# Kernel tuning notes

Measured on AMD Instinct MI355X. Metric: run time of the kernel, lower is better.

The kernel has to match this reference:

```python
import jax, jax.numpy as jnp
import numpy as np

HIDDEN = 2048
HEAD_DIM = 128
GROUPS = 8
HEADS = HIDDEN // HEAD_DIM          # 16
HPG = HEADS // GROUPS               # heads per group = 2


def setup_inputs() -> dict:
    key = jax.random.key(0)
    ks = jax.random.split(key, 9)
    b, sl, sk = 2, 2048, 2048
    s = 0.02
    return {
        "q": jax.random.normal(ks[0], (b, sl, HIDDEN), jnp.float32),
        "k": jax.random.normal(ks[1], (b, sk, HIDDEN), jnp.float32),
        "v": jax.random.normal(ks[2], (b, sk, HIDDEN), jnp.float32),
        "Wq": jax.random.normal(ks[3], (HIDDEN, HIDDEN), jnp.float32) * s,
        "bq": jax.random.normal(ks[4], (HIDDEN,), jnp.float32) * s,
        "Wk": jax.random.normal(ks[5], (HIDDEN, HEAD_DIM * GROUPS), jnp.float32) * s,
        "bk": jax.random.normal(ks[6], (HEAD_DIM * GROUPS,), jnp.float32) * s,
        "Wv": jax.random.normal(ks[7], (HIDDEN, HEAD_DIM * GROUPS), jnp.float32) * s,
        "bv": jax.random.normal(ks[8], (HEAD_DIM * GROUPS,), jnp.float32) * s,
    }


def reference(q, k, v, Wq, bq, Wk, bk, Wv, bv):
    b, sl, _ = q.shape
    sk = k.shape[1]
    qp = q @ Wq + bq                                   # [b, sl, hidden]
    kp = k @ Wk + bk                                   # [b, sk, G*d]
    vp = v @ Wv + bv                                   # [b, sk, G*d]
    # head h = g*HPG + j uses group g, matching torch repeat_interleave on dim=1
    qh = qp.reshape(b, sl, GROUPS, HPG, HEAD_DIM).transpose(0, 2, 3, 1, 4)  # [b,G,hpg,sl,d]
    kh = kp.reshape(b, sk, GROUPS, HEAD_DIM).transpose(0, 2, 1, 3)          # [b,G,sk,d]
    vh = vp.reshape(b, sk, GROUPS, HEAD_DIM).transpose(0, 2, 1, 3)          # [b,G,sk,d]
    scale = 1.0 / jnp.sqrt(jnp.asarray(HEAD_DIM, qh.dtype))
    score = jnp.einsum("bghld,bgsd->bghls", qh, kh) * scale                 # [b,G,hpg,sl,sk]
    attn = jax.nn.softmax(score, axis=-1)
    out = jnp.einsum("bghls,bgsd->bghld", attn, vh)                         # [b,G,hpg,sl,d]
    out = out.transpose(0, 3, 1, 2, 4).reshape(b, sl, HIDDEN)
    return out
```

## Files before the change

### kernel.cpp

```cpp
#include <hip/hip_runtime.h>

typedef unsigned short u16;
typedef short v8s __attribute__((ext_vector_type(8)));
typedef float v4f __attribute__((ext_vector_type(4)));
typedef float v16f __attribute__((ext_vector_type(16)));

typedef __attribute__((address_space(3))) u16* lptr_t;
typedef const __attribute__((address_space(1))) void* gptr_t;

__device__ __forceinline__ u16 f2b(float f) {
  unsigned int u = __float_as_uint(f);
  u += 0x7fff + ((u >> 16) & 1);
  return (u16)(u >> 16);
}

__global__ __launch_bounds__(256) void conv3_bf16(const float* __restrict__ q,
                                                  const float* __restrict__ k,
                                                  const float* __restrict__ v,
                                                  u16* __restrict__ qd,
                                                  u16* __restrict__ kd,
                                                  u16* __restrict__ vd) {
  int blk = blockIdx.x;
  const float* s; u16* d;
  if (blk < 4096)      { s = q; d = qd; }
  else if (blk < 8192) { s = k; d = kd; blk -= 4096; }
  else                 { s = v; d = vd; blk -= 8192; }
  int i = (blk * 256 + threadIdx.x) * 8;
  float4 a = *(const float4*)&s[i];
  float4 b = *(const float4*)&s[i + 4];
  union { uint4 v4; u16 u[8]; } p;
  p.u[0] = f2b(a.x); p.u[1] = f2b(a.y); p.u[2] = f2b(a.z); p.u[3] = f2b(a.w);
  p.u[4] = f2b(b.x); p.u[5] = f2b(b.y); p.u[6] = f2b(b.z); p.u[7] = f2b(b.w);
  *(uint4*)&d[i] = p.v4;
}

__global__ __launch_bounds__(256) void transp3_w(const float* __restrict__ Wq,
                                                 const float* __restrict__ Wk,
                                                 const float* __restrict__ Wv,
                                                 u16* __restrict__ wt) {
  __shared__ u16 tile[64][65];
  int blk = blockIdx.x;
  const float* W; int N; u16* dst;
  if (blk < 1024)      { W = Wq; N = 2048; dst = wt; }
  else if (blk < 1536) { W = Wk; N = 1024; dst = wt + (size_t)2048 * 2048; blk -= 1024; }
  else                 { W = Wv; N = 1024; dst = wt + (size_t)3072 * 2048; blk -= 1536; }
  const int k0 = (blk & 31) * 64;
  const int n0 = (blk >> 5) * 64;
  const int t = threadIdx.x;
#pragma unroll
  for (int i = 0; i < 2; ++i) {
    int chunk = i * 256 + t;
    int kr = chunk >> 3;
    int nc = (chunk & 7) * 8;
    float4 a = *(const float4*)&W[(size_t)(k0 + kr) * N + n0 + nc];
    float4 b = *(const float4*)&W[(size_t)(k0 + kr) * N + n0 + nc + 4];
    tile[kr][nc + 0] = f2b(a.x); tile[kr][nc + 1] = f2b(a.y);
    tile[kr][nc + 2] = f2b(a.z); tile[kr][nc + 3] = f2b(a.w);
    tile[kr][nc + 4] = f2b(b.x); tile[kr][nc + 5] = f2b(b.y);
    tile[kr][nc + 6] = f2b(b.z); tile[kr][nc + 7] = f2b(b.w);
  }
  __syncthreads();
#pragma unroll
  for (int i = 0; i < 2; ++i) {
    int chunk = i * 256 + t;
    int nr = chunk >> 3;
    int kc = (chunk & 7) * 8;
    union { uint4 v; u16 u[8]; } cv;
#pragma unroll
    for (int j = 0; j < 8; ++j) cv.u[j] = tile[kc + j][nr];
    *(uint4*)&dst[(size_t)(n0 + nr) * 2048 + k0 + kc] = cv.v;
  }
}

__global__ __launch_bounds__(256) void qkv_gemm(const u16* __restrict__ qbf,
                                                const u16* __restrict__ kbf,
                                                const u16* __restrict__ vbf,
                                                const u16* __restrict__ wt_all,
                                                const float* __restrict__ bq,
                                                const float* __restrict__ bk,
                                                const float* __restrict__ bv,
                                                u16* __restrict__ qp,
                                                u16* __restrict__ kp,
                                                u16* __restrict__ vpt) {
  __shared__ __align__(16) u16 A_sh[128 * 32];
  __shared__ __align__(16) u16 B_sh[128 * 32];
  const int m0 = blockIdx.x * 128;
  const int n0 = blockIdx.y * 128;
  const int t = threadIdx.x;
  const int wave = t >> 6, lane = t & 63;
  const int quad = lane >> 4, l16 = lane & 15;
  const int wm = (wave & 1) * 64, wn = (wave >> 1) * 64;

  const u16* Abase; const float* bias; int region, nloc0;
  if (n0 < 2048)      { Abase = qbf; bias = bq; region = 0; nloc0 = n0; }
  else if (n0 < 3072) { Abase = kbf; bias = bk; region = 1; nloc0 = n0 - 2048; }
  else                { Abase = vbf; bias = bv; region = 2; nloc0 = n0 - 3072; }

  const int st_r = lane >> 2;
  const int st_c = (lane & 3) * 8;
  const int seg = wave * 2;

  v4f acc[4][4] = {};

  for (int k0 = 0; k0 < 2048; k0 += 32) {
#pragma unroll
    for (int i = 0; i < 2; ++i) {
      int rows = (seg + i) * 16;
      const u16* ga = &Abase[(size_t)(m0 + rows + st_r) * 2048 + k0 + st_c];
      lptr_t la = (lptr_t)&A_sh[rows * 32] + lane * 8;
      __builtin_amdgcn_global_load_lds((gptr_t)ga,
                                       (__attribute__((address_space(3))) void*)la, 16, 0, 0);
      const u16* gb = &wt_all[(size_t)(n0 + rows + st_r) * 2048 + k0 + st_c];
      lptr_t lb = (lptr_t)&B_sh[rows * 32] + lane * 8;
      __builtin_amdgcn_global_load_lds((gptr_t)gb,
                                       (__attribute__((address_space(3))) void*)lb, 16, 0, 0);
    }
    __syncthreads();

    v8s af[4], bf[4];
#pragma unroll
    for (int i = 0; i < 4; ++i)
      af[i] = *(const v8s*)&A_sh[(wm + i * 16 + l16) * 32 + quad * 8];
#pragma unroll
    for (int j = 0; j < 4; ++j)
      bf[j] = *(const v8s*)&B_sh[(wn + j * 16 + l16) * 32 + quad * 8];
#pragma unroll
    for (int i = 0; i < 4; ++i)
#pragma unroll
      for (int j = 0; j < 4; ++j)
        acc[i][j] = __builtin_amdgcn_mfma_f32_16x16x32_bf16(af[i], bf[j], acc[i][j], 0, 0, 0);
    __syncthreads();
  }

#pragma unroll
  for (int j = 0; j < 4; ++j) {
    int nl = nloc0 + wn + j * 16 + l16;
    float bvl = bias[nl];
    if (region == 0) {
#pragma unroll
      for (int i = 0; i < 4; ++i)
#pragma unroll
        for (int r = 0; r < 4; ++r) {
          int m = m0 + wm + i * 16 + quad * 4 + r;
          qp[(size_t)m * 2048 + nl] = f2b((acc[i][j][r] + bvl) * 0.08838834764831845f);
        }
    } else if (region == 1) {
#pragma unroll
      for (int i = 0; i < 4; ++i)
#pragma unroll
        for (int r = 0; r < 4; ++r) {
          int m = m0 + wm + i * 16 + quad * 4 + r;
          kp[(size_t)m * 1024 + nl] = f2b(acc[i][j][r] + bvl);
        }
    } else {
      int g = nl >> 7, d = nl & 127;
#pragma unroll
      for (int i = 0; i < 4; ++i) {
        int mb = m0 + wm + i * 16 + quad * 4;
        int b = mb >> 11, s = mb & 2047;
        ushort4 pk;
        pk.x = f2b(acc[i][j][0] + bvl);
        pk.y = f2b(acc[i][j][1] + bvl);
        pk.z = f2b(acc[i][j][2] + bvl);
        pk.w = f2b(acc[i][j][3] + bvl);
        *(ushort4*)&vpt[(((size_t)b * 8 + g) * 128 + d) * 2048 + s] = pk;
      }
    }
  }
}

__global__ __launch_bounds__(256, 2) void gqa_attn2(const u16* __restrict__ qp,
                                                    const u16* __restrict__ kp,
                                                    const u16* __restrict__ vpt,
                                                    float* __restrict__ out) {
  __shared__ __align__(16) u16 K_sh[2][64 * 128];
  __shared__ __align__(16) u16 V_sh[2][128 * 64];

  const int qtile = blockIdx.x;
  const int head = blockIdx.y;
  const int batch = blockIdx.z;
  const int g = head >> 1;
  const int q0 = qtile * 128;

  const u16* qpb = qp + (size_t)batch * 2048 * 2048;
  const u16* kpb = kp + (size_t)batch * 2048 * 1024;
  const u16* vptb = vpt + (size_t)batch * 8 * 128 * 2048;
  float* outb = out + (size_t)batch * 2048 * 2048;

  const int t = threadIdx.x;
  const int wave = t >> 6, lane = t & 63;
  const int l = lane & 31, h = lane >> 5;

  v8s qf[8];
  {
    const u16* qrow = &qpb[(size_t)(q0 + wave * 32 + l) * 2048 + head * 128];
#pragma unroll
    for (int ks = 0; ks < 8; ++ks)
      qf[ks] = *(const v8s*)&qrow[ks * 16 + h * 8];
  }

  int colK[8];
#pragma unroll
  for (int ks = 0; ks < 8; ++ks) colK[ks] = ((2 * ks + h) ^ (l & 7)) * 8;

  int koff[4], voff[4];
#pragma unroll
  for (int i = 0; i < 4; ++i) {
    int krow = wave * 16 + i * 4 + (lane >> 4);
    int kg = (lane & 15) ^ (krow & 7);
    koff[i] = krow * 1024 + g * 128 + kg * 8;
    int vrow = wave * 32 + i * 8 + (lane >> 3);
    int vg = (lane & 7) ^ (vrow & 7);
    voff[i] = (g * 128 + vrow) * 2048 + vg * 8;
  }

#define STAGE_KV(BUF, S0)                                                               \
  do {                                                                                  \
    _Pragma("unroll") for (int i_ = 0; i_ < 4; ++i_) {                                  \
      const u16* gk_ = kpb + (size_t)(S0) * 1024 + koff[i_];                            \
      lptr_t lk_ = (lptr_t)&K_sh[BUF][(wave * 16 + i_ * 4) * 128] + lane * 8;           \
      __builtin_amdgcn_global_load_lds((gptr_t)gk_,                                     \
                                       (__attribute__((address_space(3))) void*)lk_,    \
                                       16, 0, 0);                                       \
      const u16* gv_ = vptb + voff[i_] + (S0);                                          \
      lptr_t lv_ = (lptr_t)&V_sh[BUF][(wave * 32 + i_ * 8) * 64] + lane * 8;            \
      __builtin_amdgcn_global_load_lds((gptr_t)gv_,                                     \
                                       (__attribute__((address_space(3))) void*)lv_,    \
                                       16, 0, 0);                                       \
    }                                                                                   \
  } while (0)

  v16f o_acc[4] = {};
  float rs = 0.0f;

  STAGE_KV(0, 0);
  __syncthreads();

  int cur = 0;
  for (int sc = 0; sc < 32; ++sc) {
    if (sc < 31) STAGE_KV(cur ^ 1, (sc + 1) * 64);

    v16f sacc[2] = {};
    __builtin_amdgcn_s_setprio(1);
#pragma unroll
    for (int kb = 0; kb < 2; ++kb)
#pragma unroll
      for (int ks = 0; ks < 8; ++ks) {
        v8s kf = *(const v8s*)&K_sh[cur][(kb * 32 + l) * 128 + colK[ks]];
        sacc[kb] = __builtin_amdgcn_mfma_f32_32x32x16_bf16(kf, qf[ks], sacc[kb], 0, 0, 0);
      }
    __builtin_amdgcn_s_setprio(0);

    unsigned int w[16];
#pragma unroll
    for (int kb = 0; kb < 2; ++kb)
#pragma unroll
      for (int p = 0; p < 8; ++p) {
        float e0 = __expf(sacc[kb][2 * p]);
        float e1 = __expf(sacc[kb][2 * p + 1]);
        rs += e0 + e1;
        asm("v_cvt_pk_bf16_f32 %0, %1, %2" : "=v"(w[kb * 8 + p]) : "v"(e0), "v"(e1));
      }

    v8s pa[4];
#pragma unroll
    for (int j = 0; j < 4; ++j) {
      unsigned int a = w[j * 4 + 0], c = w[j * 4 + 1];
      unsigned int b = w[j * 4 + 2], d = w[j * 4 + 3];
      asm("v_permlane32_swap_b32 %0, %1" : "+v"(a), "+v"(b));
      asm("v_permlane32_swap_b32 %0, %1" : "+v"(c), "+v"(d));
      union { unsigned int u[4]; v8s s; } pk;
      pk.u[0] = a; pk.u[1] = c; pk.u[2] = b; pk.u[3] = d;
      pa[j] = pk.s;
    }

    __builtin_amdgcn_s_setprio(1);
#pragma unroll
    for (int j = 0; j < 4; ++j)
#pragma unroll
      for (int db = 0; db < 4; ++db) {
        v8s vf = *(const v8s*)&V_sh[cur][(db * 32 + l) * 64 + colK[j]];
        o_acc[db] = __builtin_amdgcn_mfma_f32_32x32x16_bf16(pa[j], vf, o_acc[db], 0, 0, 0);
      }
    __builtin_amdgcn_s_setprio(0);

    __syncthreads();
    cur ^= 1;
  }

  float rst = rs + __shfl_xor(rs, 32, 64);
  float inv = 1.0f / rst;
#pragma unroll
  for (int r = 0; r < 16; ++r) {
    int qpat = (r & 3) + 8 * (r >> 2) + 4 * h;
    float invq = __shfl(inv, qpat, 64);
    int qrow = q0 + wave * 32 + qpat;
    float* orow = &outb[(size_t)qrow * 2048 + head * 128 + l];
#pragma unroll
    for (int db = 0; db < 4; ++db)
      orow[db * 32] = o_acc[db][r] * invq;
  }
#undef STAGE_KV
}

extern "C" void kernel_launch(void* const* d_in, const int* in_sizes, int n_in,
                              void* d_out, int out_size, void* d_ws, size_t ws_size,
                              hipStream_t stream) {
  const float* q  = (const float*)d_in[0];
  const float* k  = (const float*)d_in[1];
  const float* v  = (const float*)d_in[2];
  const float* Wq = (const float*)d_in[3];
  const float* bq = (const float*)d_in[4];
  const float* Wk = (const float*)d_in[5];
  const float* bk = (const float*)d_in[6];
  const float* Wv = (const float*)d_in[7];
  const float* bv = (const float*)d_in[8];
  float* out = (float*)d_out;
  char* ws = (char*)d_ws;

  u16* qbf    = (u16*)(ws + 0);
  u16* kbf    = (u16*)(ws + 16777216);
  u16* vbf    = (u16*)(ws + 33554432);
  u16* wt_all = (u16*)(ws + 50331648);
  u16* qp     = (u16*)(ws + 67108864);
  u16* kp     = (u16*)(ws + 83886080);
  u16* vpt    = (u16*)(ws + 92274688);

  conv3_bf16<<<12288, 256, 0, stream>>>(q, k, v, qbf, kbf, vbf);
  transp3_w<<<2048, 256, 0, stream>>>(Wq, Wk, Wv, wt_all);
  qkv_gemm<<<dim3(32, 32), 256, 0, stream>>>(qbf, kbf, vbf, wt_all,
                                             bq, bk, bv, qp, kp, vpt);
  gqa_attn2<<<dim3(16, 16, 2), 256, 0, stream>>>(qp, kp, vpt, out);
}
```

Baseline: 334.9 us.

## Rewrite QKV GEMM as 256x256 8-wave double-buffered pipelined kernel

Replaces the 128x128, 4-wave, single-buffered QKV projection GEMM with a 256x256-tile, 8-wave kernel. It double-buffers LDS with 64-wide K slices, XOR-swizzles the LDS layout, and interleaves async global-to-LDS loads with MFMA phases using explicit barriers, waitcnts and priority hints. It also remaps block IDs for L2 locality. The larger tile raises arithmetic intensity and hides load latency, at the cost of more LDS and registers, and only 256 blocks on the device.

```diff
diff --git a/kernel.cpp b/kernel.cpp
--- a/kernel.cpp
+++ b/kernel.cpp
@@ -72,98 +72,192 @@
   }
 }
 
-__global__ __launch_bounds__(256) void qkv_gemm(const u16* __restrict__ qbf,
-                                                const u16* __restrict__ kbf,
-                                                const u16* __restrict__ vbf,
-                                                const u16* __restrict__ wt_all,
-                                                const float* __restrict__ bq,
-                                                const float* __restrict__ bk,
-                                                const float* __restrict__ bv,
-                                                u16* __restrict__ qp,
-                                                u16* __restrict__ kp,
-                                                u16* __restrict__ vpt) {
-  __shared__ __align__(16) u16 A_sh[128 * 32];
-  __shared__ __align__(16) u16 B_sh[128 * 32];
-  const int m0 = blockIdx.x * 128;
-  const int n0 = blockIdx.y * 128;
+__global__ __launch_bounds__(512, 2) void qkv_gemm8(const u16* __restrict__ qbf,
+                                                    const u16* __restrict__ kbf,
+                                                    const u16* __restrict__ vbf,
+                                                    const u16* __restrict__ wt_all,
+                                                    const float* __restrict__ bq,
+                                                    const float* __restrict__ bk,
+                                                    const float* __restrict__ bv,
+                                                    u16* __restrict__ qp,
+                                                    u16* __restrict__ kp,
+                                                    u16* __restrict__ vpt) {
+  __shared__ __align__(16) u16 A_sh[2][16384];
+  __shared__ __align__(16) u16 B_sh[2][16384];
+
+  const int bid = blockIdx.x;
+  const int wg = (bid & 7) * 32 + (bid >> 3);
+  const int m0 = (wg >> 4) * 256;
+  const int n0 = (wg & 15) * 256;
+
   const int t = threadIdx.x;
-  const int wave = t >> 6, lane = t & 63;
+  const int w = t >> 6, lane = t & 63;
   const int quad = lane >> 4, l16 = lane & 15;
-  const int wm = (wave & 1) * 64, wn = (wave >> 1) * 64;
+  const int wr = w >> 2, wc = w & 3;
 
   const u16* Abase; const float* bias; int region, nloc0;
   if (n0 < 2048)      { Abase = qbf; bias = bq; region = 0; nloc0 = n0; }
   else if (n0 < 3072) { Abase = kbf; bias = bk; region = 1; nloc0 = n0 - 2048; }
   else                { Abase = vbf; bias = bv; region = 2; nloc0 = n0 - 3072; }
 
-  const int st_r = lane >> 2;
-  const int st_c = (lane & 3) * 8;
-  const int seg = wave * 2;
-
-  v4f acc[4][4] = {};
-
-  for (int k0 = 0; k0 < 2048; k0 += 32) {
-#pragma unroll
-    for (int i = 0; i < 2; ++i) {
-      int rows = (seg + i) * 16;
-      const u16* ga = &Abase[(size_t)(m0 + rows + st_r) * 2048 + k0 + st_c];
-      lptr_t la = (lptr_t)&A_sh[rows * 32] + lane * 8;
-      __builtin_amdgcn_global_load_lds((gptr_t)ga,
-                                       (__attribute__((address_space(3))) void*)la, 16, 0, 0);
-      const u16* gb = &wt_all[(size_t)(n0 + rows + st_r) * 2048 + k0 + st_c];
-      lptr_t lb = (lptr_t)&B_sh[rows * 32] + lane * 8;
-      __builtin_amdgcn_global_load_lds((gptr_t)gb,
-                                       (__attribute__((address_space(3))) void*)lb, 16, 0, 0);
+  const u16* GA = Abase + (size_t)m0 * 2048;
+  const u16* GB = wt_all + (size_t)n0 * 2048;
+
+  int offA[2][2], ldsA[2][2], offB[2][2], ldsB[2][2];
+#pragma unroll
+  for (int s_ = 0; s_ < 2; ++s_)
+#pragma unroll
+    for (int j = 0; j < 2; ++j) {
+      int r0a = j * 128 + s_ * 64 + w * 8;
+      int ra = r0a + (lane >> 3);
+      offA[s_][j] = ra * 2048 + (((lane & 7) ^ (((ra >> 2) & 1) << 1)) << 3);
+      ldsA[s_][j] = r0a * 64 + lane * 8;
+      int r0b = j * 128 + s_ * 32 + (w >> 2) * 64 + (w & 3) * 8;
+      int rb = r0b + (lane >> 3);
+      offB[s_][j] = rb * 2048 + (((lane & 7) ^ (((rb >> 2) & 1) << 1)) << 3);
+      ldsB[s_][j] = r0b * 64 + lane * 8;
     }
-    __syncthreads();
-
-    v8s af[4], bf[4];
-#pragma unroll
-    for (int i = 0; i < 4; ++i)
-      af[i] = *(const v8s*)&A_sh[(wm + i * 16 + l16) * 32 + quad * 8];
-#pragma unroll
-    for (int j = 0; j < 4; ++j)
-      bf[j] = *(const v8s*)&B_sh[(wn + j * 16 + l16) * 32 + quad * 8];
-#pragma unroll
-    for (int i = 0; i < 4; ++i)
-#pragma unroll
-      for (int j = 0; j < 4; ++j)
-        acc[i][j] = __builtin_amdgcn_mfma_f32_16x16x32_bf16(af[i], bf[j], acc[i][j], 0, 0, 0);
-    __syncthreads();
-  }
-
-#pragma unroll
-  for (int j = 0; j < 4; ++j) {
-    int nl = nloc0 + wn + j * 16 + l16;
+
+  int colK[2];
+#pragma unroll
+  for (int kk = 0; kk < 2; ++kk)
+    colK[kk] = (kk * 32 + quad * 8) ^ (((l16 >> 2) & 1) << 4);
+
+#define ST_A(BUF, KEL, S_)                                                              \
+  do {                                                                                  \
+    _Pragma("unroll") for (int j_ = 0; j_ < 2; ++j_) {                                  \
+      const u16* g_ = GA + (KEL) + offA[S_][j_];                                        \
+      lptr_t l_ = (lptr_t)&A_sh[BUF][ldsA[S_][j_]];                                     \
+      __builtin_amdgcn_global_load_lds((gptr_t)g_,                                      \
+                                       (__attribute__((address_space(3))) void*)l_,     \
+                                       16, 0, 0);                                       \
+    }                                                                                   \
+  } while (0)
+
+#define ST_B(BUF, KEL, S_)                                                              \
+  do {                                                                                  \
+    _Pragma("unroll") for (int j_ = 0; j_ < 2; ++j_) {                                  \
+      const u16* g_ = GB + (KEL) + offB[S_][j_];                                        \
+      lptr_t l_ = (lptr_t)&B_sh[BUF][ldsB[S_][j_]];                                     \
+      __builtin_amdgcn_global_load_lds((gptr_t)g_,                                      \
+                                       (__attribute__((address_space(3))) void*)l_,     \
+                                       16, 0, 0);                                       \
+    }                                                                                   \
+  } while (0)
+
+#define RD_A(BUF, MS)                                                                   \
+  do {                                                                                  \
+    const int rb_ = wr * 128 + (MS) * 64;                                               \
+    _Pragma("unroll") for (int m_ = 0; m_ < 4; ++m_)                                    \
+    _Pragma("unroll") for (int kk_ = 0; kk_ < 2; ++kk_)                                 \
+      a[m_][kk_] = *(const v8s*)&A_sh[BUF][(rb_ + m_ * 16 + l16) * 64 + colK[kk_]];     \
+  } while (0)
+
+#define RD_B(BUF, NS)                                                                   \
+  do {                                                                                  \
+    const int rb_ = wc * 64 + (NS) * 32;                                                \
+    _Pragma("unroll") for (int n_ = 0; n_ < 2; ++n_)                                    \
+    _Pragma("unroll") for (int kk_ = 0; kk_ < 2; ++kk_)                                 \
+      b[n_][kk_] = *(const v8s*)&B_sh[BUF][(rb_ + n_ * 16 + l16) * 64 + colK[kk_]];     \
+  } while (0)
+
+#define MM(MS, NS)                                                                      \
+  do {                                                                                  \
+    __builtin_amdgcn_s_setprio(1);                                                      \
+    _Pragma("unroll") for (int kk_ = 0; kk_ < 2; ++kk_)                                 \
+    _Pragma("unroll") for (int m_ = 0; m_ < 4; ++m_)                                    \
+    _Pragma("unroll") for (int n_ = 0; n_ < 2; ++n_)                                    \
+      acc[(MS) * 4 + m_][(NS) * 2 + n_] = __builtin_amdgcn_mfma_f32_16x16x32_bf16(      \
+          a[m_][kk_], b[n_][kk_], acc[(MS) * 4 + m_][(NS) * 2 + n_], 0, 0, 0);          \
+    __builtin_amdgcn_s_setprio(0);                                                      \
+  } while (0)
+
+#define PHASE_MID()                                                                     \
+  do {                                                                                  \
+    asm volatile("" ::: "memory");                                                      \
+    __builtin_amdgcn_s_barrier();                                                       \
+    asm volatile("s_waitcnt lgkmcnt(0)" ::: "memory");                                  \
+    __builtin_amdgcn_sched_barrier(0);                                                  \
+  } while (0)
+
+#define PHASE_END()                                                                     \
+  do {                                                                                  \
+    asm volatile("" ::: "memory");                                                      \
+    __builtin_amdgcn_s_barrier();                                                       \
+    __builtin_amdgcn_sched_barrier(0);                                                  \
+  } while (0)
+
+#define PHASE_END_V()                                                                   \
+  do {                                                                                  \
+    asm volatile("s_waitcnt vmcnt(6)" ::: "memory");                                    \
+    __builtin_amdgcn_s_barrier();                                                       \
+    __builtin_amdgcn_sched_barrier(0);                                                  \
+  } while (0)
+
+  v4f acc[8][4] = {};
+  v8s a[4][2], b[2][2];
+
+  ST_A(0, 0, 0); ST_B(0, 0, 0); ST_A(0, 0, 1); ST_B(0, 0, 1);
+  ST_B(1, 64, 0); ST_A(1, 64, 1); ST_B(1, 64, 1);
+  asm volatile("s_waitcnt vmcnt(6)" ::: "memory");
+  __builtin_amdgcn_s_barrier();
+  __builtin_amdgcn_sched_barrier(0);
+
+  for (int it = 0; it < 16; ++it) {
+    const int k1 = (2 * it + 1) * 64;
+    const int k2 = ((2 * it + 2) & 31) * 64;
+    const int k3 = ((2 * it + 3) & 31) * 64;
+    RD_A(0, 0); RD_B(0, 0); ST_A(1, k1, 0); PHASE_MID(); MM(0, 0); PHASE_END();
+    RD_A(0, 1);             ST_B(0, k2, 0); PHASE_MID(); MM(1, 0); PHASE_END();
+    RD_B(0, 1);             ST_A(0, k2, 1); PHASE_MID(); MM(1, 1); PHASE_END();
+    RD_A(0, 0);             ST_B(0, k2, 1); PHASE_MID(); MM(0, 1); PHASE_END_V();
+    RD_A(1, 0); RD_B(1, 0); ST_A(0, k2, 0); PHASE_MID(); MM(0, 0); PHASE_END();
+    RD_A(1, 1);             ST_B(1, k3, 0); PHASE_MID(); MM(1, 0); PHASE_END();
+    RD_B(1, 1);             ST_A(1, k3, 1); PHASE_MID(); MM(1, 1); PHASE_END();
+    RD_A(1, 0);             ST_B(1, k3, 1); PHASE_MID(); MM(0, 1); PHASE_END_V();
+  }
+
+#undef ST_A
+#undef ST_B
+#undef RD_A
+#undef RD_B
+#undef MM
+#undef PHASE_MID
+#undef PHASE_END
+#undef PHASE_END_V
+
+#pragma unroll
+  for (int n = 0; n < 4; ++n) {
+    int nl = nloc0 + wc * 64 + n * 16 + l16;
     float bvl = bias[nl];
     if (region == 0) {
 #pragma unroll
-      for (int i = 0; i < 4; ++i)
+      for (int m = 0; m < 8; ++m)
 #pragma unroll
         for (int r = 0; r < 4; ++r) {
-          int m = m0 + wm + i * 16 + quad * 4 + r;
-          qp[(size_t)m * 2048 + nl] = f2b((acc[i][j][r] + bvl) * 0.08838834764831845f);
+          int mg = m0 + wr * 128 + m * 16 + quad * 4 + r;
+          qp[(size_t)mg * 2048 + nl] = f2b((acc[m][n][r] + bvl) * 0.08838834764831845f);
         }
     } else if (region == 1) {
 #pragma unroll
-      for (int i = 0; i < 4; ++i)
+      for (int m = 0; m < 8; ++m)
 #pragma unroll
         for (int r = 0; r < 4; ++r) {
-          int m = m0 + wm + i * 16 + quad * 4 + r;
-          kp[(size_t)m * 1024 + nl] = f2b(acc[i][j][r] + bvl);
+          int mg = m0 + wr * 128 + m * 16 + quad * 4 + r;
+          kp[(size_t)mg * 1024 + nl] = f2b(acc[m][n][r] + bvl);
         }
     } else {
       int g = nl >> 7, d = nl & 127;
 #pragma unroll
-      for (int i = 0; i < 4; ++i) {
-        int mb = m0 + wm + i * 16 + quad * 4;
-        int b = mb >> 11, s = mb & 2047;
+      for (int m = 0; m < 8; ++m) {
+        int mb = m0 + wr * 128 + m * 16 + quad * 4;
+        int bb = mb >> 11, s = mb & 2047;
         ushort4 pk;
-        pk.x = f2b(acc[i][j][0] + bvl);
-        pk.y = f2b(acc[i][j][1] + bvl);
-        pk.z = f2b(acc[i][j][2] + bvl);
-        pk.w = f2b(acc[i][j][3] + bvl);
-        *(ushort4*)&vpt[(((size_t)b * 8 + g) * 128 + d) * 2048 + s] = pk;
+        pk.x = f2b(acc[m][n][0] + bvl);
+        pk.y = f2b(acc[m][n][1] + bvl);
+        pk.z = f2b(acc[m][n][2] + bvl);
+        pk.w = f2b(acc[m][n][3] + bvl);
+        *(ushort4*)&vpt[(((size_t)bb * 8 + g) * 128 + d) * 2048 + s] = pk;
       }
     }
   }
@@ -251,7 +345,7 @@
       }
     __builtin_amdgcn_s_setprio(0);
 
-    unsigned int w[16];
+    unsigned int wv[16];
 #pragma unroll
     for (int kb = 0; kb < 2; ++kb)
 #pragma unroll
@@ -259,14 +353,14 @@
         float e0 = __expf(sacc[kb][2 * p]);
         float e1 = __expf(sacc[kb][2 * p + 1]);
         rs += e0 + e1;
-        asm("v_cvt_pk_bf16_f32 %0, %1, %2" : "=v"(w[kb * 8 + p]) : "v"(e0), "v"(e1));
+        asm("v_cvt_pk_bf16_f32 %0, %1, %2" : "=v"(wv[kb * 8 + p]) : "v"(e0), "v"(e1));
       }
 
     v8s pa[4];
 #pragma unroll
     for (int j = 0; j < 4; ++j) {
-      unsigned int a = w[j * 4 + 0], c = w[j * 4 + 1];
-      unsigned int b = w[j * 4 + 2], d = w[j * 4 + 3];
+      unsigned int a = wv[j * 4 + 0], c = wv[j * 4 + 1];
+      unsigned int b = wv[j * 4 + 2], d = wv[j * 4 + 3];
       asm("v_permlane32_swap_b32 %0, %1" : "+v"(a), "+v"(b));
       asm("v_permlane32_swap_b32 %0, %1" : "+v"(c), "+v"(d));
       union { unsigned int u[4]; v8s s; } pk;
@@ -328,7 +422,7 @@
 
   conv3_bf16<<<12288, 256, 0, stream>>>(q, k, v, qbf, kbf, vbf);
   transp3_w<<<2048, 256, 0, stream>>>(Wq, Wk, Wv, wt_all);
-  qkv_gemm<<<dim3(32, 32), 256, 0, stream>>>(qbf, kbf, vbf, wt_all,
-                                             bq, bk, bv, qp, kp, vpt);
+  qkv_gemm8<<<256, 512, 0, stream>>>(qbf, kbf, vbf, wt_all,
+                                     bq, bk, bv, qp, kp, vpt);
   gqa_attn2<<<dim3(16, 16, 2), 256, 0, stream>>>(qp, kp, vpt, out);
 }
```

Measured after the change: 338.0 us. Within noise of the previous version (+0.9%).
